# Performance work log

Hardware: AMD Instinct MI355X
Metric: run time of the kernel (lower is better)

Reference implementation:

```python
import jax, jax.numpy as jnp
import numpy as np


def setup_inputs() -> dict:
    key = jax.random.key(0)
    k1, k2, k3 = jax.random.split(key, 3)
    B, C, H, W = 16, 32, 48, 48
    inp = jax.random.normal(k1, (B, C, H, W), dtype=jnp.float32)
    # weight channels encode a CxC matrix per pixel; add identity (in the
    # flattened C*C channel layout) so every per-pixel matrix is well
    # conditioned for solve/slogdet, as a trained flow's weights would be.
    w = jax.random.normal(k2, (B, C * C, H, W), dtype=jnp.float32) * 0.1
    eye = jnp.eye(C, dtype=jnp.float32).reshape(C * C, 1, 1)
    w = w + eye
    logdet = jax.random.normal(k3, (B,), dtype=jnp.float32)
    return {"input": inp, "weight": w, "logdet": logdet}


def reference(input, weight, logdet):
    # forward (reverse=False) path of InvConditionalLinear
    B, C, H, W = input.shape
    # [B, C*C, H, W] -> [B, H, W, C, C] per-pixel matrices
    w = jnp.transpose(weight, (0, 2, 3, 1)).reshape(B, H, W, C, C)
    # sum of per-pixel log|det W| over all pixels -> [B]
    weight_logdet = jnp.sum(jnp.linalg.slogdet(w)[1], axis=(1, 2))
    # batched per-pixel solve: W z = x
    rhs = jnp.transpose(input, (0, 2, 3, 1))[..., None]  # [B,H,W,C,1]
    z = jnp.linalg.solve(w, rhs)[..., 0]                  # [B,H,W,C]
    z = jnp.transpose(z, (0, 3, 1, 2))                    # [B,C,H,W]
    return z, logdet - weight_logdet
```

## Files before the change

kernel.cpp:

```cpp
#include <hip/hip_runtime.h>
#include <math.h>

#define CDIM 32
#define HWDIM 2304
#define BDIM 16
#define PPW 8
#define NTHREADS 256
#define PPB 32
#define ZOFF (BDIM * CDIM * HWDIM)

__device__ __forceinline__ void gload_lds16(const float* g, float* l) {
    __builtin_amdgcn_global_load_lds(
        (const __attribute__((address_space(1))) float*)g,
        (__attribute__((address_space(3))) float*)l, 16, 0, 0);
}

__global__ __launch_bounds__(NTHREADS, 2)
void solve_kernel(const float* __restrict__ input,
                  const float* __restrict__ weight,
                  const float* __restrict__ logdet,
                  float* __restrict__ out) {
    const int t    = threadIdx.x;
    const int lane = t & 63;
    const int wv   = t >> 6;
    const int h    = lane & 7;
    const int p    = lane >> 3;
    const int gb   = lane & 56;

    const int blk  = blockIdx.x;
    const int b    = blk / (HWDIM / PPB);
    const int pb   = (blk % (HWDIM / PPB)) * PPB;
    const int pixl = wv * PPW + p;
    const int pix0 = pb + wv * PPW;
    const int pix  = pb + pixl;

    __shared__ float lds[2][256 * CDIM];

    const float* xp = input + (size_t)b * CDIM * HWDIM + (size_t)h * HWDIM + pix;
    float y[4];
    #pragma unroll
    for (int r = 0; r < 4; ++r) y[r] = xp[(size_t)(r * 8) * HWDIM];
    asm volatile("" ::: "memory");

    const int sg = lane >> 3;
    const int sp = lane & 7;
    const int ps = pixl >> 2, pc = pixl & 3;
    const float* wbase = weight + (size_t)b * (CDIM * CDIM) * HWDIM + pb;
    const float* srcA = wbase + (size_t)(wv * 64 + sg) * HWDIM
                              + ((sp ^ (2 * wv)) << 2);
    const float* srcB = wbase + (size_t)(wv * 64 + sg) * HWDIM
                              + ((sp ^ (2 * wv + 1)) << 2);

    auto stage = [&](int r, int buf) {
        float* lbase = &lds[buf][(wv * 64) * CDIM];
        #pragma unroll
        for (int q = 0; q < 8; ++q) {
            const float* s = (q < 4 ? srcA : srcB)
                           + (size_t)(r * 256 + q * 8) * HWDIM;
            gload_lds16(s, lbase + q * 8 * CDIM);
        }
    };

    stage(0, 0);
    asm volatile("" ::: "memory");
    stage(1, 1);

    float A[4][CDIM];
    #pragma unroll
    for (int r = 0; r < 4; ++r) {
        if (r < 3) asm volatile("s_waitcnt vmcnt(8)" ::: "memory");
        else       asm volatile("s_waitcnt vmcnt(0)" ::: "memory");
        __builtin_amdgcn_s_barrier();
        asm volatile("" ::: "memory");
        #pragma unroll
        for (int j = 0; j < CDIM; ++j)
            A[r][j] = lds[r & 1][(h * CDIM + j) * CDIM + ((ps ^ h) << 2) + pc];
        if (r < 2) {
            asm volatile("s_waitcnt lgkmcnt(0)" ::: "memory");
            __builtin_amdgcn_s_barrier();
            asm volatile("" ::: "memory");
            stage(r + 2, r & 1);
        }
    }

    float lacc = 0.0f;
    #pragma unroll
    for (int k = 0; k < CDIM; ++k) {
        const int tr = k >> 3, k7 = k & 7;
        const int src = gb + k7;
        float bp = __shfl(A[tr][k], src);
        float r  = __builtin_amdgcn_rcpf(bp);
        lacc += __log2f(fabsf(bp));

        float m[4];
        m[tr] = (h > k7) ? A[tr][k] * r : ((h == k7) ? (1.0f - r) : 0.0f);
        #pragma unroll
        for (int q = tr + 1; q < 4; ++q) m[q] = A[q][k] * r;

        #pragma unroll
        for (int j = k + 1; j < CDIM; ++j) {
            float bv = __shfl(A[tr][j], src);
            #pragma unroll
            for (int q = tr; q < 4; ++q)
                A[q][j] = fmaf(-m[q], bv, A[q][j]);
        }
        float bq = __shfl(y[tr], src);
        #pragma unroll
        for (int q = tr; q < 4; ++q) y[q] = fmaf(-m[q], bq, y[q]);
    }

    #pragma unroll
    for (int k = CDIM - 1; k >= 1; --k) {
        const int tr = k >> 3, k7 = k & 7;
        const int src = gb + k7;
        float bz = __shfl(y[tr], src);
        float c = (h < k7) ? A[tr][k] : 0.0f;
        y[tr] = fmaf(-c, bz, y[tr]);
        #pragma unroll
        for (int q = 0; q < tr; ++q)
            y[q] = fmaf(-A[q][k], bz, y[q]);
    }

    float* zp = out + (size_t)b * CDIM * HWDIM + (size_t)h * HWDIM + pix;
    #pragma unroll
    for (int r = 0; r < 4; ++r) zp[(size_t)(r * 8) * HWDIM] = y[r];

    float v2 = lacc;
    v2 += __shfl_xor(v2, 8);
    v2 += __shfl_xor(v2, 16);
    v2 += __shfl_xor(v2, 32);
    if (lane == 0) {
        float add = -v2 * 0.69314718055994531f;
        if (pix0 == 0) add += logdet[b];
        atomicAdd(&out[ZOFF + b], add);
    }
}

extern "C" void kernel_launch(void* const* d_in, const int* in_sizes, int n_in,
                              void* d_out, int out_size, void* d_ws, size_t ws_size,
                              hipStream_t stream) {
    const float* input  = (const float*)d_in[0];
    const float* weight = (const float*)d_in[1];
    const float* logdet = (const float*)d_in[2];
    float* out = (float*)d_out;

    solve_kernel<<<BDIM * (HWDIM / PPB), NTHREADS, 0, stream>>>(input, weight,
                                                                logdet, out);
}
```

Before: 258.8 us.

## Halve LDS staging chunk to raise occupancy with eight-chunk pipeline

```diff
diff --git a/kernel.cpp b/kernel.cpp
--- a/kernel.cpp
+++ b/kernel.cpp
@@ -7,6 +7,8 @@
 #define PPW 8
 #define NTHREADS 256
 #define PPB 32
+#define CROWS 128
+#define NCHUNK 8
 #define ZOFF (BDIM * CDIM * HWDIM)
 
 __device__ __forceinline__ void gload_lds16(const float* g, float* l) {
@@ -15,7 +17,7 @@
         (__attribute__((address_space(3))) float*)l, 16, 0, 0);
 }
 
-__global__ __launch_bounds__(NTHREADS, 2)
+__global__ __launch_bounds__(NTHREADS, 5)
 void solve_kernel(const float* __restrict__ input,
                   const float* __restrict__ weight,
                   const float* __restrict__ logdet,
@@ -34,7 +36,7 @@
     const int pix0 = pb + wv * PPW;
     const int pix  = pb + pixl;
 
-    __shared__ float lds[2][256 * CDIM];
+    __shared__ float lds[2][CROWS * CDIM];
 
     const float* xp = input + (size_t)b * CDIM * HWDIM + (size_t)h * HWDIM + pix;
     float y[4];
@@ -46,18 +48,14 @@
     const int sp = lane & 7;
     const int ps = pixl >> 2, pc = pixl & 3;
     const float* wbase = weight + (size_t)b * (CDIM * CDIM) * HWDIM + pb;
-    const float* srcA = wbase + (size_t)(wv * 64 + sg) * HWDIM
-                              + ((sp ^ (2 * wv)) << 2);
-    const float* srcB = wbase + (size_t)(wv * 64 + sg) * HWDIM
-                              + ((sp ^ (2 * wv + 1)) << 2);
+    const float* src = wbase + (size_t)(wv * 32 + sg) * HWDIM + ((sp ^ wv) << 2);
 
     auto stage = [&](int r, int buf) {
-        float* lbase = &lds[buf][(wv * 64) * CDIM];
+        float* lbase = &lds[buf][(wv * 32) * CDIM];
         #pragma unroll
-        for (int q = 0; q < 8; ++q) {
-            const float* s = (q < 4 ? srcA : srcB)
-                           + (size_t)(r * 256 + q * 8) * HWDIM;
-            gload_lds16(s, lbase + q * 8 * CDIM);
+        for (int q = 0; q < 4; ++q) {
+            gload_lds16(src + (size_t)(r * CROWS + q * 8) * HWDIM,
+                        lbase + q * 8 * CDIM);
         }
     };
 
@@ -67,15 +65,19 @@
 
     float A[4][CDIM];
     #pragma unroll
-    for (int r = 0; r < 4; ++r) {
-        if (r < 3) asm volatile("s_waitcnt vmcnt(8)" ::: "memory");
-        else       asm volatile("s_waitcnt vmcnt(0)" ::: "memory");
+    for (int r = 0; r < NCHUNK; ++r) {
+        if (r < NCHUNK - 1) asm volatile("s_waitcnt vmcnt(4)" ::: "memory");
+        else                asm volatile("s_waitcnt vmcnt(0)" ::: "memory");
         __builtin_amdgcn_s_barrier();
         asm volatile("" ::: "memory");
-        #pragma unroll
-        for (int j = 0; j < CDIM; ++j)
-            A[r][j] = lds[r & 1][(h * CDIM + j) * CDIM + ((ps ^ h) << 2) + pc];
-        if (r < 2) {
+        if ((h >> 2) == (r & 1)) {
+            const int rr = r >> 1;
+            #pragma unroll
+            for (int j = 0; j < CDIM; ++j)
+                A[rr][j] = lds[r & 1][((h & 3) * CDIM + j) * CDIM
+                                      + ((ps ^ (h & 3)) << 2) + pc];
+        }
+        if (r < NCHUNK - 2) {
             asm volatile("s_waitcnt lgkmcnt(0)" ::: "memory");
             __builtin_amdgcn_s_barrier();
             asm volatile("" ::: "memory");
@@ -87,8 +89,8 @@
     #pragma unroll
     for (int k = 0; k < CDIM; ++k) {
         const int tr = k >> 3, k7 = k & 7;
-        const int src = gb + k7;
-        float bp = __shfl(A[tr][k], src);
+        const int srcl = gb + k7;
+        float bp = __shfl(A[tr][k], srcl);
         float r  = __builtin_amdgcn_rcpf(bp);
         lacc += __log2f(fabsf(bp));
 
@@ -99,12 +101,12 @@
 
         #pragma unroll
         for (int j = k + 1; j < CDIM; ++j) {
-            float bv = __shfl(A[tr][j], src);
+            float bv = __shfl(A[tr][j], srcl);
             #pragma unroll
             for (int q = tr; q < 4; ++q)
                 A[q][j] = fmaf(-m[q], bv, A[q][j]);
         }
-        float bq = __shfl(y[tr], src);
+        float bq = __shfl(y[tr], srcl);
         #pragma unroll
         for (int q = tr; q < 4; ++q) y[q] = fmaf(-m[q], bq, y[q]);
     }
@@ -112,8 +114,8 @@
     #pragma unroll
     for (int k = CDIM - 1; k >= 1; --k) {
         const int tr = k >> 3, k7 = k & 7;
-        const int src = gb + k7;
-        float bz = __shfl(y[tr], src);
+        const int srcl = gb + k7;
+        float bz = __shfl(y[tr], srcl);
         float c = (h < k7) ? A[tr][k] : 0.0f;
         y[tr] = fmaf(-c, bz, y[tr]);
         #pragma unroll
```

New measurement: 413.7 us. +59.9%, slower.

## Factor LU via LDS pivot-row broadcast, then DPP-based forward/back substitution

Applied to the files above, without the earlier changes.

```diff
diff --git a/kernel.cpp b/kernel.cpp
--- a/kernel.cpp
+++ b/kernel.cpp
@@ -7,12 +7,36 @@
 #define PPW 8
 #define NTHREADS 256
 #define PPB 32
+#define CROWS 256
 #define ZOFF (BDIM * CDIM * HWDIM)
 
 __device__ __forceinline__ void gload_lds16(const float* g, float* l) {
     __builtin_amdgcn_global_load_lds(
         (const __attribute__((address_space(1))) float*)g,
         (__attribute__((address_space(3))) float*)l, 16, 0, 0);
+}
+
+__device__ __forceinline__ float bcast8(float x, int k7) {
+    int v = __float_as_int(x), b;
+    switch (k7) {
+    case 0: b = __builtin_amdgcn_update_dpp(v, v, 0x00, 0xF, 0xF, false);
+            b = __builtin_amdgcn_update_dpp(b, b, 0x114, 0xF, 0xA, false); break;
+    case 1: b = __builtin_amdgcn_update_dpp(v, v, 0x55, 0xF, 0xF, false);
+            b = __builtin_amdgcn_update_dpp(b, b, 0x114, 0xF, 0xA, false); break;
+    case 2: b = __builtin_amdgcn_update_dpp(v, v, 0xAA, 0xF, 0xF, false);
+            b = __builtin_amdgcn_update_dpp(b, b, 0x114, 0xF, 0xA, false); break;
+    case 3: b = __builtin_amdgcn_update_dpp(v, v, 0xFF, 0xF, 0xF, false);
+            b = __builtin_amdgcn_update_dpp(b, b, 0x114, 0xF, 0xA, false); break;
+    case 4: b = __builtin_amdgcn_update_dpp(v, v, 0x00, 0xF, 0xF, false);
+            b = __builtin_amdgcn_update_dpp(b, b, 0x104, 0xF, 0x5, false); break;
+    case 5: b = __builtin_amdgcn_update_dpp(v, v, 0x55, 0xF, 0xF, false);
+            b = __builtin_amdgcn_update_dpp(b, b, 0x104, 0xF, 0x5, false); break;
+    case 6: b = __builtin_amdgcn_update_dpp(v, v, 0xAA, 0xF, 0xF, false);
+            b = __builtin_amdgcn_update_dpp(b, b, 0x104, 0xF, 0x5, false); break;
+    default: b = __builtin_amdgcn_update_dpp(v, v, 0xFF, 0xF, 0xF, false);
+            b = __builtin_amdgcn_update_dpp(b, b, 0x104, 0xF, 0x5, false); break;
+    }
+    return __int_as_float(b);
 }
 
 __global__ __launch_bounds__(NTHREADS, 2)
@@ -25,7 +49,6 @@
     const int wv   = t >> 6;
     const int h    = lane & 7;
     const int p    = lane >> 3;
-    const int gb   = lane & 56;
 
     const int blk  = blockIdx.x;
     const int b    = blk / (HWDIM / PPB);
@@ -34,7 +57,8 @@
     const int pix0 = pb + wv * PPW;
     const int pix  = pb + pixl;
 
-    __shared__ float lds[2][256 * CDIM];
+    __shared__ float lds[2][CROWS * CDIM];
+    __shared__ __align__(16) float ubuf[PPB][36];
 
     const float* xp = input + (size_t)b * CDIM * HWDIM + (size_t)h * HWDIM + pix;
     float y[4];
@@ -83,42 +107,71 @@
         }
     }
 
+    float* ub = ubuf[pixl];
+    float rr[4] = {0.0f, 0.0f, 0.0f, 0.0f};
     float lacc = 0.0f;
+
+    #pragma unroll
+    for (int k = 0; k < CDIM; ++k) {
+        const int tr = k >> 3, k7 = k & 7, q0 = k >> 2;
+        if (h == k7) {
+            #pragma unroll
+            for (int j = k; j < CDIM; ++j) ub[j] = A[tr][j];
+        }
+        asm volatile("s_waitcnt lgkmcnt(0)" ::: "memory");
+        float4 bv4[8];
+        #pragma unroll
+        for (int qq = 0; qq < 8; ++qq)
+            if (qq >= q0)
+                bv4[qq] = *reinterpret_cast<const float4*>(&ub[qq * 4]);
+
+        const float piv  = reinterpret_cast<const float*>(&bv4[q0])[k & 3];
+        const float rcpv = __builtin_amdgcn_rcpf(piv);
+        lacc += __log2f(fabsf(piv));
+        rr[tr] = (h == k7) ? rcpv : rr[tr];
+
+        float m[4];
+        #pragma unroll
+        for (int q = 0; q < 4; ++q) {
+            if (q < tr)       m[q] = 0.0f;
+            else if (q == tr) m[q] = (h > k7) ? A[tr][k] * rcpv : 0.0f;
+            else              m[q] = A[q][k] * rcpv;
+        }
+        A[tr][k] = (h > k7) ? m[tr] : A[tr][k];
+        #pragma unroll
+        for (int q = tr + 1; q < 4; ++q) A[q][k] = m[q];
+
+        #pragma unroll
+        for (int j = k + 1; j < CDIM; ++j) {
+            const float bvj = reinterpret_cast<const float*>(&bv4[j >> 2])[j & 3];
+            #pragma unroll
+            for (int q = tr; q < 4; ++q)
+                A[q][j] = fmaf(-m[q], bvj, A[q][j]);
+        }
+    }
+
     #pragma unroll
     for (int k = 0; k < CDIM; ++k) {
         const int tr = k >> 3, k7 = k & 7;
-        const int src = gb + k7;
-        float bp = __shfl(A[tr][k], src);
-        float r  = __builtin_amdgcn_rcpf(bp);
-        lacc += __log2f(fabsf(bp));
-
-        float m[4];
-        m[tr] = (h > k7) ? A[tr][k] * r : ((h == k7) ? (1.0f - r) : 0.0f);
-        #pragma unroll
-        for (int q = tr + 1; q < 4; ++q) m[q] = A[q][k] * r;
-
-        #pragma unroll
-        for (int j = k + 1; j < CDIM; ++j) {
-            float bv = __shfl(A[tr][j], src);
+        float bq = bcast8(y[tr], k7);
+        float mk = (h > k7) ? A[tr][k] : 0.0f;
+        y[tr] = fmaf(-mk, bq, y[tr]);
+        #pragma unroll
+        for (int q = tr + 1; q < 4; ++q) y[q] = fmaf(-A[q][k], bq, y[q]);
+    }
+
+    #pragma unroll
+    for (int k = CDIM - 1; k >= 0; --k) {
+        const int tr = k >> 3, k7 = k & 7;
+        y[tr] = (h == k7) ? y[tr] * rr[tr] : y[tr];
+        if (k > 0) {
+            float bz = bcast8(y[tr], k7);
+            float cm = (h < k7) ? A[tr][k] : 0.0f;
+            y[tr] = fmaf(-cm, bz, y[tr]);
             #pragma unroll
-            for (int q = tr; q < 4; ++q)
-                A[q][j] = fmaf(-m[q], bv, A[q][j]);
-        }
-        float bq = __shfl(y[tr], src);
-        #pragma unroll
-        for (int q = tr; q < 4; ++q) y[q] = fmaf(-m[q], bq, y[q]);
-    }
-
-    #pragma unroll
-    for (int k = CDIM - 1; k >= 1; --k) {
-        const int tr = k >> 3, k7 = k & 7;
-        const int src = gb + k7;
-        float bz = __shfl(y[tr], src);
-        float c = (h < k7) ? A[tr][k] : 0.0f;
-        y[tr] = fmaf(-c, bz, y[tr]);
-        #pragma unroll
-        for (int q = 0; q < tr; ++q)
-            y[q] = fmaf(-A[q][k], bz, y[q]);
+            for (int q = 0; q < tr; ++q)
+                y[q] = fmaf(-A[q][k], bz, y[q]);
+        }
     }
 
     float* zp = out + (size_t)b * CDIM * HWDIM + (size_t)h * HWDIM + pix;
```

New measurement: 634.4 us. 145% more time.

## Split each pixel's matrix over 16 lanes with DPP broadcasts and left-looking LU

Applied to the files above, without the earlier changes.

```diff
diff --git a/kernel.cpp b/kernel.cpp
--- a/kernel.cpp
+++ b/kernel.cpp
@@ -4,8 +4,7 @@
 #define CDIM 32
 #define HWDIM 2304
 #define BDIM 16
-#define PPW 8
-#define NTHREADS 256
+#define NTHREADS 512
 #define PPB 32
 #define ZOFF (BDIM * CDIM * HWDIM)
 
@@ -15,118 +14,139 @@
         (__attribute__((address_space(3))) float*)l, 16, 0, 0);
 }
 
-__global__ __launch_bounds__(NTHREADS, 2)
+__device__ __forceinline__ float bcast16(float x, int k15) {
+    int v = __float_as_int(x), b;
+    switch (k15 & 3) {
+    case 0:  b = __builtin_amdgcn_update_dpp(v, v, 0x00, 0xF, 0xF, false); break;
+    case 1:  b = __builtin_amdgcn_update_dpp(v, v, 0x55, 0xF, 0xF, false); break;
+    case 2:  b = __builtin_amdgcn_update_dpp(v, v, 0xAA, 0xF, 0xF, false); break;
+    default: b = __builtin_amdgcn_update_dpp(v, v, 0xFF, 0xF, 0xF, false); break;
+    }
+    switch (k15 >> 2) {
+    case 0:
+        b = __builtin_amdgcn_update_dpp(b, b, 0x114, 0xF, 0x2, false);
+        b = __builtin_amdgcn_update_dpp(b, b, 0x118, 0xF, 0xC, false); break;
+    case 1:
+        b = __builtin_amdgcn_update_dpp(b, b, 0x104, 0xF, 0x1, false);
+        b = __builtin_amdgcn_update_dpp(b, b, 0x118, 0xF, 0xC, false); break;
+    case 2:
+        b = __builtin_amdgcn_update_dpp(b, b, 0x114, 0xF, 0x8, false);
+        b = __builtin_amdgcn_update_dpp(b, b, 0x108, 0xF, 0x3, false); break;
+    default:
+        b = __builtin_amdgcn_update_dpp(b, b, 0x104, 0xF, 0x4, false);
+        b = __builtin_amdgcn_update_dpp(b, b, 0x108, 0xF, 0x3, false); break;
+    }
+    return __int_as_float(b);
+}
+
+__global__ __launch_bounds__(NTHREADS, 4)
 void solve_kernel(const float* __restrict__ input,
                   const float* __restrict__ weight,
                   const float* __restrict__ logdet,
                   float* __restrict__ out) {
     const int t    = threadIdx.x;
     const int lane = t & 63;
-    const int wv   = t >> 6;
-    const int h    = lane & 7;
-    const int p    = lane >> 3;
-    const int gb   = lane & 56;
+    const int W8   = t >> 6;
+    const int h16  = lane & 15;
+    const int g    = lane >> 4;
 
     const int blk  = blockIdx.x;
     const int b    = blk / (HWDIM / PPB);
     const int pb   = (blk % (HWDIM / PPB)) * PPB;
-    const int pixl = wv * PPW + p;
-    const int pix0 = pb + wv * PPW;
+    const int pixl = W8 * 4 + g;
+    const int pix0 = pb + W8 * 4;
     const int pix  = pb + pixl;
 
     __shared__ float lds[2][256 * CDIM];
 
-    const float* xp = input + (size_t)b * CDIM * HWDIM + (size_t)h * HWDIM + pix;
-    float y[4];
+    const float* xp = input + (size_t)b * CDIM * HWDIM + (size_t)h16 * HWDIM + pix;
+    float y[2];
     #pragma unroll
-    for (int r = 0; r < 4; ++r) y[r] = xp[(size_t)(r * 8) * HWDIM];
+    for (int r = 0; r < 2; ++r) y[r] = xp[(size_t)(r * 16) * HWDIM];
     asm volatile("" ::: "memory");
 
     const int sg = lane >> 3;
     const int sp = lane & 7;
-    const int ps = pixl >> 2, pc = pixl & 3;
     const float* wbase = weight + (size_t)b * (CDIM * CDIM) * HWDIM + pb;
-    const float* srcA = wbase + (size_t)(wv * 64 + sg) * HWDIM
-                              + ((sp ^ (2 * wv)) << 2);
-    const float* srcB = wbase + (size_t)(wv * 64 + sg) * HWDIM
-                              + ((sp ^ (2 * wv + 1)) << 2);
+    const float* src = wbase + (size_t)(W8 * 32 + sg) * HWDIM + ((sp ^ W8) << 2);
 
-    auto stage = [&](int r, int buf) {
-        float* lbase = &lds[buf][(wv * 64) * CDIM];
+    auto stage = [&](int c, int buf) {
+        float* lbase = &lds[buf][(W8 * 32) * CDIM];
         #pragma unroll
-        for (int q = 0; q < 8; ++q) {
-            const float* s = (q < 4 ? srcA : srcB)
-                           + (size_t)(r * 256 + q * 8) * HWDIM;
-            gload_lds16(s, lbase + q * 8 * CDIM);
-        }
+        for (int q = 0; q < 4; ++q)
+            gload_lds16(src + (size_t)(c * 256 + q * 8) * HWDIM,
+                        lbase + q * 8 * CDIM);
     };
 
     stage(0, 0);
     asm volatile("" ::: "memory");
     stage(1, 1);
 
-    float A[4][CDIM];
+    float A[2][CDIM];
     #pragma unroll
-    for (int r = 0; r < 4; ++r) {
-        if (r < 3) asm volatile("s_waitcnt vmcnt(8)" ::: "memory");
+    for (int c = 0; c < 4; ++c) {
+        if (c < 3) asm volatile("s_waitcnt vmcnt(4)" ::: "memory");
         else       asm volatile("s_waitcnt vmcnt(0)" ::: "memory");
         __builtin_amdgcn_s_barrier();
         asm volatile("" ::: "memory");
-        #pragma unroll
-        for (int j = 0; j < CDIM; ++j)
-            A[r][j] = lds[r & 1][(h * CDIM + j) * CDIM + ((ps ^ h) << 2) + pc];
-        if (r < 2) {
+        if ((h16 >> 3) == (c & 1)) {
+            const int rbase = (h16 & 7) * 32;
+            const int slot  = ((W8 ^ (h16 & 7)) << 2) + g;
+            #pragma unroll
+            for (int j = 0; j < CDIM; ++j)
+                A[c >> 1][j] = lds[c & 1][(rbase + j) * 32 + slot];
+        }
+        if (c < 2) {
             asm volatile("s_waitcnt lgkmcnt(0)" ::: "memory");
             __builtin_amdgcn_s_barrier();
             asm volatile("" ::: "memory");
-            stage(r + 2, r & 1);
+            stage(c + 2, c & 1);
         }
     }
 
     float lacc = 0.0f;
     #pragma unroll
+    for (int j = 0; j < CDIM; ++j) {
+        #pragma unroll
+        for (int k = 0; k < j; ++k) {
+            const int trk = k >> 4, k15 = k & 15;
+            float bv = bcast16(A[trk][j], k15);
+            float mk = (h16 >= k15) ? A[trk][k] : 0.0f;
+            A[trk][j] = fmaf(-mk, bv, A[trk][j]);
+            if (trk == 0) A[1][j] = fmaf(-A[1][k], bv, A[1][j]);
+        }
+        const int trj = j >> 4, j15 = j & 15;
+        float bp = bcast16(A[trj][j], j15);
+        float rcpv = __builtin_amdgcn_rcpf(bp);
+        lacc += __log2f(fabsf(bp));
+        A[trj][j] = (h16 > j15) ? A[trj][j] * rcpv
+                                : ((h16 == j15) ? (1.0f - rcpv) : A[trj][j]);
+        if (trj == 0) A[1][j] *= rcpv;
+    }
+
+    #pragma unroll
     for (int k = 0; k < CDIM; ++k) {
-        const int tr = k >> 3, k7 = k & 7;
-        const int src = gb + k7;
-        float bp = __shfl(A[tr][k], src);
-        float r  = __builtin_amdgcn_rcpf(bp);
-        lacc += __log2f(fabsf(bp));
-
-        float m[4];
-        m[tr] = (h > k7) ? A[tr][k] * r : ((h == k7) ? (1.0f - r) : 0.0f);
-        #pragma unroll
-        for (int q = tr + 1; q < 4; ++q) m[q] = A[q][k] * r;
-
-        #pragma unroll
-        for (int j = k + 1; j < CDIM; ++j) {
-            float bv = __shfl(A[tr][j], src);
-            #pragma unroll
-            for (int q = tr; q < 4; ++q)
-                A[q][j] = fmaf(-m[q], bv, A[q][j]);
-        }
-        float bq = __shfl(y[tr], src);
-        #pragma unroll
-        for (int q = tr; q < 4; ++q) y[q] = fmaf(-m[q], bq, y[q]);
+        const int tr = k >> 4, k15 = k & 15;
+        float bq = bcast16(y[tr], k15);
+        float mk = (h16 >= k15) ? A[tr][k] : 0.0f;
+        y[tr] = fmaf(-mk, bq, y[tr]);
+        if (tr == 0) y[1] = fmaf(-A[1][k], bq, y[1]);
     }
 
     #pragma unroll
     for (int k = CDIM - 1; k >= 1; --k) {
-        const int tr = k >> 3, k7 = k & 7;
-        const int src = gb + k7;
-        float bz = __shfl(y[tr], src);
-        float c = (h < k7) ? A[tr][k] : 0.0f;
-        y[tr] = fmaf(-c, bz, y[tr]);
-        #pragma unroll
-        for (int q = 0; q < tr; ++q)
-            y[q] = fmaf(-A[q][k], bz, y[q]);
+        const int tr = k >> 4, k15 = k & 15;
+        float bz = bcast16(y[tr], k15);
+        float cm = (h16 < k15) ? A[tr][k] : 0.0f;
+        y[tr] = fmaf(-cm, bz, y[tr]);
+        if (tr == 1) y[0] = fmaf(-A[0][k], bz, y[0]);
     }
 
-    float* zp = out + (size_t)b * CDIM * HWDIM + (size_t)h * HWDIM + pix;
+    float* zp = out + (size_t)b * CDIM * HWDIM + (size_t)h16 * HWDIM + pix;
     #pragma unroll
-    for (int r = 0; r < 4; ++r) zp[(size_t)(r * 8) * HWDIM] = y[r];
+    for (int r = 0; r < 2; ++r) zp[(size_t)(r * 16) * HWDIM] = y[r];
 
     float v2 = lacc;
-    v2 += __shfl_xor(v2, 8);
     v2 += __shfl_xor(v2, 16);
     v2 += __shfl_xor(v2, 32);
     if (lane == 0) {
```

After: 323.3 us. 1.25x slower.
